# Kernel tuning notes

Hardware: AMD Instinct MI355X
Metric: run time of the kernel (lower is better)

## Reference

```python
import jax, jax.numpy as jnp
import numpy as np

B, S, D, NH = 4, 2048, 512, 8
HD = D // NH
SCALING = HD ** -0.5


def setup_inputs() -> dict:
    key = jax.random.key(0)
    ks = jax.random.split(key, 8)
    w_std = (2.0 / (D + D)) ** 0.5  # xavier_uniform-ish scale
    inp = {
        "query": jax.random.normal(ks[0], (B, S, D), jnp.float32),
        "key": jax.random.normal(ks[1], (B, S, D), jnp.float32),
        "value": jax.random.normal(ks[2], (B, S, D), jnp.float32),
        "key_mask": jnp.ones((B, S), dtype=bool),
        "attn_mask": jnp.tril(jnp.ones((S, S), dtype=bool)),  # causal, per docstring
        "Wq": jax.random.normal(ks[3], (D, D), jnp.float32) * w_std,
        "bq": jnp.zeros((D,), jnp.float32),
        "Wk": jax.random.normal(ks[4], (D, D), jnp.float32) * w_std,
        "bk": jnp.zeros((D,), jnp.float32),
        "Wv": jax.random.normal(ks[5], (D, D), jnp.float32) * w_std,
        "bv": jnp.zeros((D,), jnp.float32),
        "Wo": jax.random.normal(ks[6], (D, D), jnp.float32) * w_std,
        "bo": jnp.zeros((D,), jnp.float32),
    }
    return inp


def reference(query, key, value, key_mask, attn_mask, Wq, bq, Wk, bk, Wv, bv, Wo, bo):
    b, q_len, d = query.shape
    k_len = key.shape[1]
    # projections (nn.Linear: x @ W.T + b)
    q = (query @ Wq.T + bq) * SCALING
    k = key @ Wk.T + bk
    v = value @ Wv.T + bv
    q = q.reshape(b, q_len, NH, HD)
    k = k.reshape(b, k_len, NH, HD)
    v = v.reshape(b, k_len, NH, HD)
    # scores: [b, q, k, n]
    attn = jnp.einsum('bqnh,bknh->bqkn', q, k)
    # key_mask: 1 = attend; masked_fill(~mask, -inf)
    attn = jnp.where(key_mask[:, None, :, None], attn, -jnp.inf)
    # attn_mask: [q, k], 1 = attend
    attn = jnp.where(attn_mask[None, :, :, None], attn, -jnp.inf)
    attn = jax.nn.softmax(attn, axis=2)
    # dropout p=0.0 in eval -> identity
    out = jnp.einsum('bqkn,bknh->bqnh', attn, v)
    out = out.reshape(b, q_len, d)
    out = out @ Wo.T + bo
    return (out, attn)
```

## Files before the change

kernel.cpp:

```cpp
#include <hip/hip_runtime.h>


typedef short bf8 __attribute__((ext_vector_type(8)));
typedef short bf4 __attribute__((ext_vector_type(4)));
typedef float f4  __attribute__((ext_vector_type(4)));

#define MFMA16(a, b, c) __builtin_amdgcn_mfma_f32_16x16x32_bf16(a, b, c, 0, 0, 0)

static __device__ __forceinline__ short f2bf(float x) {
  unsigned u = __builtin_bit_cast(unsigned, x);
  unsigned r = (u + 0x7fffu + ((u >> 16) & 1u)) >> 16;
  return (short)r;
}
static __device__ __forceinline__ f4 zero4() { f4 z = {0.f, 0.f, 0.f, 0.f}; return z; }

template <int MODE, int INBF>
__global__ __launch_bounds__(256, 2) void gemm_proj(const void* __restrict__ Ain,
                                                    const float* __restrict__ W,
                                                    const float* __restrict__ bias,
                                                    void* __restrict__ outp, float scale) {
  __shared__ short As[128 * 40];
  __shared__ short Bs[128 * 40];
  const int tid = threadIdx.x;
  const int wave = tid >> 6, lane = tid & 63, quad = lane >> 4, col = lane & 15;
  const int m0 = blockIdx.y * 128, n0 = blockIdx.x * 128;
  const int row_off = (wave >> 1) * 64, col_off = (wave & 1) * 64;

  f4 acc[4][4];
#pragma unroll
  for (int i = 0; i < 4; ++i)
#pragma unroll
    for (int j = 0; j < 4; ++j) acc[i][j] = zero4();

  float bv[4];
#pragma unroll
  for (int nt = 0; nt < 4; ++nt) bv[nt] = bias[n0 + col_off + nt * 16 + col];

  for (int k0 = 0; k0 < 512; k0 += 32) {
#pragma unroll
    for (int i = 0; i < 4; ++i) {
      int c = i * 256 + tid;
      int r = c >> 3, cc = (c & 7) * 4;
      if constexpr (INBF) {
        const short* A = (const short*)Ain;
        *(bf4*)&As[r * 40 + cc] = *(const bf4*)(A + (size_t)(m0 + r) * 512 + k0 + cc);
      } else {
        const float* A = (const float*)Ain;
        f4 v = *(const f4*)(A + (size_t)(m0 + r) * 512 + k0 + cc);
        bf4 s = {f2bf(v[0]), f2bf(v[1]), f2bf(v[2]), f2bf(v[3])};
        *(bf4*)&As[r * 40 + cc] = s;
      }
      f4 w = *(const f4*)(W + (size_t)(n0 + r) * 512 + k0 + cc);
      bf4 sw = {f2bf(w[0]), f2bf(w[1]), f2bf(w[2]), f2bf(w[3])};
      *(bf4*)&Bs[r * 40 + cc] = sw;
    }
    __syncthreads();
    bf8 af[4], bw[4];
#pragma unroll
    for (int mt = 0; mt < 4; ++mt) af[mt] = *(const bf8*)&As[(row_off + mt * 16 + col) * 40 + quad * 8];
#pragma unroll
    for (int nt = 0; nt < 4; ++nt) bw[nt] = *(const bf8*)&Bs[(col_off + nt * 16 + col) * 40 + quad * 8];
#pragma unroll
    for (int mt = 0; mt < 4; ++mt)
#pragma unroll
      for (int nt = 0; nt < 4; ++nt) acc[mt][nt] = MFMA16(af[mt], bw[nt], acc[mt][nt]);
    __syncthreads();
  }

  if constexpr (MODE == 2) {
    float* out = (float*)outp;
#pragma unroll
    for (int mt = 0; mt < 4; ++mt)
#pragma unroll
      for (int nt = 0; nt < 4; ++nt) {
        int rb = m0 + row_off + mt * 16 + quad * 4;
        int cg = n0 + col_off + nt * 16 + col;
#pragma unroll
        for (int r = 0; r < 4; ++r) out[(size_t)(rb + r) * 512 + cg] = acc[mt][nt][r] + bv[nt];
      }
  } else {
    __shared__ short Ct[128 * 136];
#pragma unroll
    for (int mt = 0; mt < 4; ++mt)
#pragma unroll
      for (int nt = 0; nt < 4; ++nt) {
        if constexpr (MODE == 0) {
#pragma unroll
          for (int r = 0; r < 4; ++r)
            Ct[(row_off + mt * 16 + quad * 4 + r) * 136 + col_off + nt * 16 + col] =
                f2bf((acc[mt][nt][r] + bv[nt]) * scale);
        } else {
          bf4 s = {f2bf((acc[mt][nt][0] + bv[nt]) * scale), f2bf((acc[mt][nt][1] + bv[nt]) * scale),
                   f2bf((acc[mt][nt][2] + bv[nt]) * scale), f2bf((acc[mt][nt][3] + bv[nt]) * scale)};
          *(bf4*)&Ct[(col_off + nt * 16 + col) * 136 + row_off + mt * 16 + quad * 4] = s;
        }
      }
    __syncthreads();
    short* out = (short*)outp;
#pragma unroll
    for (int it = 0; it < 8; ++it) {
      int c = it * 256 + tid;
      if constexpr (MODE == 0) {
        int row = c >> 4, ch = (c & 15) * 8;
        int m = m0 + row, bb = m >> 11, sidx = m & 2047;
        int cg = n0 + ch, n = cg >> 6, h = cg & 63;
        bf8 v = *(const bf8*)&Ct[row * 136 + ch];
        *(bf8*)(out + ((size_t)((bb * 8 + n) * 2048 + sidx)) * 64 + h) = v;
      } else {
        int j = c >> 4, sc8 = (c & 15) * 8;
        int cg = n0 + j, n = cg >> 6, h = cg & 63;
        int m = m0 + sc8, bb = m >> 11, srow = m & 2047;
        bf8 v = *(const bf8*)&Ct[j * 136 + sc8];
        *(bf8*)(out + ((size_t)((bb * 8 + n) * 64 + h)) * 2048 + srow) = v;
      }
    }
  }
}

__global__ __launch_bounds__(512, 4) void attn_k(const short* __restrict__ Q,
                                                 const short* __restrict__ K,
                                                 const short* __restrict__ Vt,
                                                 short* __restrict__ O,
                                                 float* __restrict__ attn) {
  __shared__ float Pl[16 * 516];
  const int tid = threadIdx.x;
  const int wv = tid >> 6, lane = tid & 63, quad = lane >> 4, col = lane & 15;
  const int bid = blockIdx.x;
  const int b = bid & 3;
  const int q0 = (127 - (bid >> 2)) * 16;
  const int q_hi = q0 + 15;
  const int nsteps = (q_hi >> 6) + 1;

  const size_t hb = (size_t)(b * 8 + wv) * 2048;
  const bf8 aq0 = *(const bf8*)(Q + (hb + q0 + col) * 64 + quad * 8);
  const bf8 aq1 = *(const bf8*)(Q + (hb + q0 + col) * 64 + 32 + quad * 8);

  float rl[4] = {0.f, 0.f, 0.f, 0.f};

  for (int ks = 0; ks < nsteps; ++ks) {
    int k0 = ks << 6;
#pragma unroll
    for (int kt = 0; kt < 4; ++kt) {
      int kb = k0 + kt * 16;
      if (kb <= q_hi) {
        const short* kp = K + (hb + kb + col) * 64 + quad * 8;
        bf8 b0 = *(const bf8*)kp;
        bf8 b1 = *(const bf8*)(kp + 32);
        f4 sc = zero4();
        sc = MFMA16(aq0, b0, sc);
        sc = MFMA16(aq1, b1, sc);
        if (kb + 15 <= q0) {
#pragma unroll
          for (int r = 0; r < 4; ++r) rl[r] += __expf(sc[r]);
        } else {
          int kg = kb + col;
#pragma unroll
          for (int r = 0; r < 4; ++r) rl[r] += (kg <= q0 + quad * 4 + r) ? __expf(sc[r]) : 0.f;
        }
      }
    }
  }
#pragma unroll
  for (int r = 0; r < 4; ++r) {
    float v = rl[r];
    v += __shfl_xor(v, 1);
    v += __shfl_xor(v, 2);
    v += __shfl_xor(v, 4);
    v += __shfl_xor(v, 8);
    rl[r] = 1.0f / v;
  }

  f4 oacc[4];
#pragma unroll
  for (int t = 0; t < 4; ++t) oacc[t] = zero4();

  for (int ks = 0; ks < nsteps; ++ks) {
    int k0 = ks << 6;
#pragma unroll
    for (int kt = 0; kt < 4; ++kt) {
      int kb = k0 + kt * 16;
      f4 p = zero4();
      if (kb <= q_hi) {
        const short* kp = K + (hb + kb + col) * 64 + quad * 8;
        bf8 b0 = *(const bf8*)kp;
        bf8 b1 = *(const bf8*)(kp + 32);
        f4 sc = zero4();
        sc = MFMA16(aq0, b0, sc);
        sc = MFMA16(aq1, b1, sc);
        if (kb + 15 <= q0) {
#pragma unroll
          for (int r = 0; r < 4; ++r) p[r] = __expf(sc[r]) * rl[r];
        } else {
          int kg = kb + col;
#pragma unroll
          for (int r = 0; r < 4; ++r)
            p[r] = (kg <= q0 + quad * 4 + r) ? __expf(sc[r]) * rl[r] : 0.f;
        }
      }
      int kl = kt * 16 + col;
#pragma unroll
      for (int r = 0; r < 4; ++r) Pl[(quad * 4 + r) * 516 + kl * 8 + wv] = p[r];
    }
    __syncthreads();
    {
      int q = tid >> 5, c0 = tid & 31;
      float* dst = attn + ((size_t)(b * 2048 + q0 + q) * 2048 + k0) * 8;
      const float* src = Pl + q * 516;
#pragma unroll
      for (int i = 0; i < 4; ++i) {
        int cc = (c0 + 32 * i) * 4;
        *(f4*)(dst + cc) = *(const f4*)(src + cc);
      }
    }
#pragma unroll
    for (int kk = 0; kk < 2; ++kk) {
      const float* pp = Pl + col * 516 + (kk * 32 + quad * 8) * 8 + wv;
      bf8 ap;
#pragma unroll
      for (int j = 0; j < 8; ++j) ap[j] = f2bf(pp[j * 8]);
#pragma unroll
      for (int t = 0; t < 4; ++t) {
        const short* vp = Vt + ((size_t)((b * 8 + wv) * 64 + t * 16 + col)) * 2048 + k0 + kk * 32 + quad * 8;
        bf8 bvv = *(const bf8*)vp;
        oacc[t] = MFMA16(ap, bvv, oacc[t]);
      }
    }
    __syncthreads();
  }

  int klim = nsteps << 6;
  if (klim < 2048) {
    int nf4 = (2048 - klim) * 2;
#pragma unroll 1
    for (int qq = 0; qq < 16; ++qq) {
      f4* dst = (f4*)(attn + ((size_t)(b * 2048 + q0 + qq) * 2048 + klim) * 8);
      for (int i = tid; i < nf4; i += 512) dst[i] = zero4();
    }
  }

#pragma unroll
  for (int t = 0; t < 4; ++t)
#pragma unroll
    for (int r = 0; r < 4; ++r) Pl[(quad * 4 + r) * 516 + wv * 64 + t * 16 + col] = oacc[t][r];
  __syncthreads();
  {
    int q = tid >> 5, c0 = tid & 31;
    const float* src = Pl + q * 516;
    short* dst = O + (size_t)(b * 2048 + q0 + q) * 512;
#pragma unroll
    for (int i = 0; i < 4; ++i) {
      int cc = (c0 + 32 * i) * 4;
      f4 v = *(const f4*)(src + cc);
      bf4 s = {f2bf(v[0]), f2bf(v[1]), f2bf(v[2]), f2bf(v[3])};
      *(bf4*)(dst + cc) = s;
    }
  }
}

extern "C" void kernel_launch(void* const* d_in, const int* in_sizes, int n_in,
                              void* d_out, int out_size, void* d_ws, size_t ws_size,
                              hipStream_t stream) {
  const float* query = (const float*)d_in[0];
  const float* key = (const float*)d_in[1];
  const float* value = (const float*)d_in[2];
  const float* Wq = (const float*)d_in[5];
  const float* bq = (const float*)d_in[6];
  const float* Wk = (const float*)d_in[7];
  const float* bk = (const float*)d_in[8];
  const float* Wv = (const float*)d_in[9];
  const float* bv = (const float*)d_in[10];
  const float* Wo = (const float*)d_in[11];
  const float* bo = (const float*)d_in[12];

  char* ws = (char*)d_ws;
  const size_t MB8 = (size_t)8 * 1024 * 1024;
  short* Qb = (short*)(ws);
  short* Kb = (short*)(ws + MB8);
  short* Vt = (short*)(ws + 2 * MB8);
  short* Ob = (short*)(ws + 3 * MB8);

  float* out = (float*)d_out;
  float* attn = out + (size_t)4 * 2048 * 512;

  dim3 g(4, 64);
  gemm_proj<0, 0><<<g, 256, 0, stream>>>((const void*)query, Wq, bq, (void*)Qb, 0.125f);
  gemm_proj<0, 0><<<g, 256, 0, stream>>>((const void*)key, Wk, bk, (void*)Kb, 1.0f);
  gemm_proj<1, 0><<<g, 256, 0, stream>>>((const void*)value, Wv, bv, (void*)Vt, 1.0f);
  attn_k<<<512, 512, 0, stream>>>(Qb, Kb, Vt, Ob, attn);
  gemm_proj<2, 1><<<g, 256, 0, stream>>>((const void*)Ob, Wo, bo, (void*)out, 1.0f);
}
```

Measured before the change: 883.4 us.

## Batch QKV projections into one launch and restructure attention P staging layout

Merges the three Q/K/V projection GEMMs into a single launch using blockIdx.z, giving one larger grid instead of three small sequential kernels. In the attention kernel, P is now staged per-head in padded LDS slabs, so the MFMA A-operand can be read with vector loads. Softmax normalisation is moved out of the inner loop: it is applied to the attention-probability store and to the final output accumulator. The huge attention-probability tensor is written with nontemporal stores. The new LDS layout makes the global write gather across slabs, which may cause bank conflicts, and adds a shared array for the reciprocal row sums.

```diff
diff --git a/kernel.cpp b/kernel.cpp
--- a/kernel.cpp
+++ b/kernel.cpp
@@ -14,11 +14,111 @@
 }
 static __device__ __forceinline__ f4 zero4() { f4 z = {0.f, 0.f, 0.f, 0.f}; return z; }
 
-template <int MODE, int INBF>
-__global__ __launch_bounds__(256, 2) void gemm_proj(const void* __restrict__ Ain,
-                                                    const float* __restrict__ W,
-                                                    const float* __restrict__ bias,
-                                                    void* __restrict__ outp, float scale) {
+__global__ __launch_bounds__(256, 3) void gemm_qkv(const float* __restrict__ Aq,
+                                                   const float* __restrict__ Ak,
+                                                   const float* __restrict__ Av,
+                                                   const float* __restrict__ Wq,
+                                                   const float* __restrict__ Wk,
+                                                   const float* __restrict__ Wv,
+                                                   const float* __restrict__ bq,
+                                                   const float* __restrict__ bk,
+                                                   const float* __restrict__ bv,
+                                                   short* __restrict__ Qo,
+                                                   short* __restrict__ Ko,
+                                                   short* __restrict__ Vo) {
+  __shared__ short As[128 * 40];
+  __shared__ short Bs[128 * 40];
+  const int z = blockIdx.z;
+  const float* A = (z == 0) ? Aq : (z == 1) ? Ak : Av;
+  const float* W = (z == 0) ? Wq : (z == 1) ? Wk : Wv;
+  const float* bias = (z == 0) ? bq : (z == 1) ? bk : bv;
+  short* out = (z == 0) ? Qo : (z == 1) ? Ko : Vo;
+  const float scale = (z == 0) ? 0.125f : 1.0f;
+
+  const int tid = threadIdx.x;
+  const int wave = tid >> 6, lane = tid & 63, quad = lane >> 4, col = lane & 15;
+  const int m0 = blockIdx.y * 128, n0 = blockIdx.x * 128;
+  const int row_off = (wave >> 1) * 64, col_off = (wave & 1) * 64;
+
+  f4 acc[4][4];
+#pragma unroll
+  for (int i = 0; i < 4; ++i)
+#pragma unroll
+    for (int j = 0; j < 4; ++j) acc[i][j] = zero4();
+
+  float bvv[4];
+#pragma unroll
+  for (int nt = 0; nt < 4; ++nt) bvv[nt] = bias[n0 + col_off + nt * 16 + col];
+
+  for (int k0 = 0; k0 < 512; k0 += 32) {
+#pragma unroll
+    for (int i = 0; i < 4; ++i) {
+      int c = i * 256 + tid;
+      int r = c >> 3, cc = (c & 7) * 4;
+      f4 v = *(const f4*)(A + (size_t)(m0 + r) * 512 + k0 + cc);
+      bf4 s = {f2bf(v[0]), f2bf(v[1]), f2bf(v[2]), f2bf(v[3])};
+      *(bf4*)&As[r * 40 + cc] = s;
+      f4 w = *(const f4*)(W + (size_t)(n0 + r) * 512 + k0 + cc);
+      bf4 sw = {f2bf(w[0]), f2bf(w[1]), f2bf(w[2]), f2bf(w[3])};
+      *(bf4*)&Bs[r * 40 + cc] = sw;
+    }
+    __syncthreads();
+    bf8 af[4], bw[4];
+#pragma unroll
+    for (int mt = 0; mt < 4; ++mt) af[mt] = *(const bf8*)&As[(row_off + mt * 16 + col) * 40 + quad * 8];
+#pragma unroll
+    for (int nt = 0; nt < 4; ++nt) bw[nt] = *(const bf8*)&Bs[(col_off + nt * 16 + col) * 40 + quad * 8];
+#pragma unroll
+    for (int mt = 0; mt < 4; ++mt)
+#pragma unroll
+      for (int nt = 0; nt < 4; ++nt) acc[mt][nt] = MFMA16(af[mt], bw[nt], acc[mt][nt]);
+    __syncthreads();
+  }
+
+  __shared__ short Ct[128 * 136];
+  if (z != 2) {
+#pragma unroll
+    for (int mt = 0; mt < 4; ++mt)
+#pragma unroll
+      for (int nt = 0; nt < 4; ++nt)
+#pragma unroll
+        for (int r = 0; r < 4; ++r)
+          Ct[(row_off + mt * 16 + quad * 4 + r) * 136 + col_off + nt * 16 + col] =
+              f2bf((acc[mt][nt][r] + bvv[nt]) * scale);
+  } else {
+#pragma unroll
+    for (int mt = 0; mt < 4; ++mt)
+#pragma unroll
+      for (int nt = 0; nt < 4; ++nt) {
+        bf4 s = {f2bf(acc[mt][nt][0] + bvv[nt]), f2bf(acc[mt][nt][1] + bvv[nt]),
+                 f2bf(acc[mt][nt][2] + bvv[nt]), f2bf(acc[mt][nt][3] + bvv[nt])};
+        *(bf4*)&Ct[(col_off + nt * 16 + col) * 136 + row_off + mt * 16 + quad * 4] = s;
+      }
+  }
+  __syncthreads();
+#pragma unroll
+  for (int it = 0; it < 8; ++it) {
+    int c = it * 256 + tid;
+    if (z != 2) {
+      int row = c >> 4, ch = (c & 15) * 8;
+      int m = m0 + row, bb = m >> 11, sidx = m & 2047;
+      int cg = n0 + ch, n = cg >> 6, h = cg & 63;
+      bf8 v = *(const bf8*)&Ct[row * 136 + ch];
+      *(bf8*)(out + ((size_t)((bb * 8 + n) * 2048 + sidx)) * 64 + h) = v;
+    } else {
+      int j = c >> 4, sc8 = (c & 15) * 8;
+      int cg = n0 + j, n = cg >> 6, h = cg & 63;
+      int m = m0 + sc8, bb = m >> 11, srow = m & 2047;
+      bf8 v = *(const bf8*)&Ct[j * 136 + sc8];
+      *(bf8*)(out + ((size_t)((bb * 8 + n) * 64 + h)) * 2048 + srow) = v;
+    }
+  }
+}
+
+__global__ __launch_bounds__(256, 2) void gemm_out(const short* __restrict__ A,
+                                                   const float* __restrict__ W,
+                                                   const float* __restrict__ bias,
+                                                   float* __restrict__ out) {
   __shared__ short As[128 * 40];
   __shared__ short Bs[128 * 40];
   const int tid = threadIdx.x;
@@ -41,15 +141,7 @@
     for (int i = 0; i < 4; ++i) {
       int c = i * 256 + tid;
       int r = c >> 3, cc = (c & 7) * 4;
-      if constexpr (INBF) {
-        const short* A = (const short*)Ain;
-        *(bf4*)&As[r * 40 + cc] = *(const bf4*)(A + (size_t)(m0 + r) * 512 + k0 + cc);
-      } else {
-        const float* A = (const float*)Ain;
-        f4 v = *(const f4*)(A + (size_t)(m0 + r) * 512 + k0 + cc);
-        bf4 s = {f2bf(v[0]), f2bf(v[1]), f2bf(v[2]), f2bf(v[3])};
-        *(bf4*)&As[r * 40 + cc] = s;
-      }
+      *(bf4*)&As[r * 40 + cc] = *(const bf4*)(A + (size_t)(m0 + r) * 512 + k0 + cc);
       f4 w = *(const f4*)(W + (size_t)(n0 + r) * 512 + k0 + cc);
       bf4 sw = {f2bf(w[0]), f2bf(w[1]), f2bf(w[2]), f2bf(w[3])};
       *(bf4*)&Bs[r * 40 + cc] = sw;
@@ -67,62 +159,26 @@
     __syncthreads();
   }
 
-  if constexpr (MODE == 2) {
-    float* out = (float*)outp;
-#pragma unroll
-    for (int mt = 0; mt < 4; ++mt)
-#pragma unroll
-      for (int nt = 0; nt < 4; ++nt) {
-        int rb = m0 + row_off + mt * 16 + quad * 4;
-        int cg = n0 + col_off + nt * 16 + col;
-#pragma unroll
-        for (int r = 0; r < 4; ++r) out[(size_t)(rb + r) * 512 + cg] = acc[mt][nt][r] + bv[nt];
-      }
-  } else {
-    __shared__ short Ct[128 * 136];
-#pragma unroll
-    for (int mt = 0; mt < 4; ++mt)
-#pragma unroll
-      for (int nt = 0; nt < 4; ++nt) {
-        if constexpr (MODE == 0) {
-#pragma unroll
-          for (int r = 0; r < 4; ++r)
-            Ct[(row_off + mt * 16 + quad * 4 + r) * 136 + col_off + nt * 16 + col] =
-                f2bf((acc[mt][nt][r] + bv[nt]) * scale);
-        } else {
-          bf4 s = {f2bf((acc[mt][nt][0] + bv[nt]) * scale), f2bf((acc[mt][nt][1] + bv[nt]) * scale),
-                   f2bf((acc[mt][nt][2] + bv[nt]) * scale), f2bf((acc[mt][nt][3] + bv[nt]) * scale)};
-          *(bf4*)&Ct[(col_off + nt * 16 + col) * 136 + row_off + mt * 16 + quad * 4] = s;
-        }
-      }
-    __syncthreads();
-    short* out = (short*)outp;
-#pragma unroll
-    for (int it = 0; it < 8; ++it) {
-      int c = it * 256 + tid;
-      if constexpr (MODE == 0) {
-        int row = c >> 4, ch = (c & 15) * 8;
-        int m = m0 + row, bb = m >> 11, sidx = m & 2047;
-        int cg = n0 + ch, n = cg >> 6, h = cg & 63;
-        bf8 v = *(const bf8*)&Ct[row * 136 + ch];
-        *(bf8*)(out + ((size_t)((bb * 8 + n) * 2048 + sidx)) * 64 + h) = v;
-      } else {
-        int j = c >> 4, sc8 = (c & 15) * 8;
-        int cg = n0 + j, n = cg >> 6, h = cg & 63;
-        int m = m0 + sc8, bb = m >> 11, srow = m & 2047;
-        bf8 v = *(const bf8*)&Ct[j * 136 + sc8];
-        *(bf8*)(out + ((size_t)((bb * 8 + n) * 64 + h)) * 2048 + srow) = v;
-      }
-    }
-  }
-}
+#pragma unroll
+  for (int mt = 0; mt < 4; ++mt)
+#pragma unroll
+    for (int nt = 0; nt < 4; ++nt) {
+      int rb = m0 + row_off + mt * 16 + quad * 4;
+      int cg = n0 + col_off + nt * 16 + col;
+#pragma unroll
+      for (int r = 0; r < 4; ++r) out[(size_t)(rb + r) * 512 + cg] = acc[mt][nt][r] + bv[nt];
+    }
+}
+
+#define SLAB 1092
 
 __global__ __launch_bounds__(512, 4) void attn_k(const short* __restrict__ Q,
                                                  const short* __restrict__ K,
                                                  const short* __restrict__ Vt,
                                                  short* __restrict__ O,
                                                  float* __restrict__ attn) {
-  __shared__ float Pl[16 * 516];
+  __shared__ float Pl[8 * SLAB];
+  __shared__ float rl_s[128];
   const int tid = threadIdx.x;
   const int wv = tid >> 6, lane = tid & 63, quad = lane >> 4, col = lane & 15;
   const int bid = blockIdx.x;
@@ -136,7 +192,6 @@
   const bf8 aq1 = *(const bf8*)(Q + (hb + q0 + col) * 64 + 32 + quad * 8);
 
   float rl[4] = {0.f, 0.f, 0.f, 0.f};
-
   for (int ks = 0; ks < nsteps; ++ks) {
     int k0 = ks << 6;
 #pragma unroll
@@ -169,6 +224,17 @@
     v += __shfl_xor(v, 8);
     rl[r] = 1.0f / v;
   }
+  if (col == 0) {
+#pragma unroll
+    for (int r = 0; r < 4; ++r) rl_s[wv * 16 + quad * 4 + r] = rl[r];
+  }
+  __syncthreads();
+
+  const int gq = tid >> 5, gc0 = tid & 31;
+  const int gnb = (gc0 & 1) * 4, gk0 = gc0 >> 1;
+  float rl8[4];
+#pragma unroll
+  for (int j = 0; j < 4; ++j) rl8[j] = rl_s[(gnb + j) * 16 + gq];
 
   f4 oacc[4];
 #pragma unroll
@@ -189,35 +255,37 @@
         sc = MFMA16(aq1, b1, sc);
         if (kb + 15 <= q0) {
 #pragma unroll
-          for (int r = 0; r < 4; ++r) p[r] = __expf(sc[r]) * rl[r];
+          for (int r = 0; r < 4; ++r) p[r] = __expf(sc[r]);
         } else {
           int kg = kb + col;
 #pragma unroll
-          for (int r = 0; r < 4; ++r)
-            p[r] = (kg <= q0 + quad * 4 + r) ? __expf(sc[r]) * rl[r] : 0.f;
+          for (int r = 0; r < 4; ++r) p[r] = (kg <= q0 + quad * 4 + r) ? __expf(sc[r]) : 0.f;
         }
       }
-      int kl = kt * 16 + col;
-#pragma unroll
-      for (int r = 0; r < 4; ++r) Pl[(quad * 4 + r) * 516 + kl * 8 + wv] = p[r];
+      float* wp = Pl + wv * SLAB + (quad * 4) * 68 + kt * 16 + col;
+#pragma unroll
+      for (int r = 0; r < 4; ++r) wp[r * 68] = p[r];
     }
     __syncthreads();
     {
-      int q = tid >> 5, c0 = tid & 31;
-      float* dst = attn + ((size_t)(b * 2048 + q0 + q) * 2048 + k0) * 8;
-      const float* src = Pl + q * 516;
+      float* dst = attn + ((size_t)(b * 2048 + q0 + gq) * 2048 + k0) * 8;
+      const float* base = Pl + gq * 68;
 #pragma unroll
       for (int i = 0; i < 4; ++i) {
-        int cc = (c0 + 32 * i) * 4;
-        *(f4*)(dst + cc) = *(const f4*)(src + cc);
+        int k = gk0 + 16 * i;
+        f4 v;
+#pragma unroll
+        for (int j = 0; j < 4; ++j) v[j] = base[(gnb + j) * SLAB + k] * rl8[j];
+        __builtin_nontemporal_store(v, (f4*)(dst + k * 8 + gnb));
       }
     }
 #pragma unroll
     for (int kk = 0; kk < 2; ++kk) {
-      const float* pp = Pl + col * 516 + (kk * 32 + quad * 8) * 8 + wv;
-      bf8 ap;
-#pragma unroll
-      for (int j = 0; j < 8; ++j) ap[j] = f2bf(pp[j * 8]);
+      const float* pp = Pl + wv * SLAB + col * 68 + kk * 32 + quad * 8;
+      f4 a0 = *(const f4*)pp;
+      f4 a1 = *(const f4*)(pp + 4);
+      bf8 ap = {f2bf(a0[0]), f2bf(a0[1]), f2bf(a0[2]), f2bf(a0[3]),
+                f2bf(a1[0]), f2bf(a1[1]), f2bf(a1[2]), f2bf(a1[3])};
 #pragma unroll
       for (int t = 0; t < 4; ++t) {
         const short* vp = Vt + ((size_t)((b * 8 + wv) * 64 + t * 16 + col)) * 2048 + k0 + kk * 32 + quad * 8;
@@ -234,22 +302,22 @@
 #pragma unroll 1
     for (int qq = 0; qq < 16; ++qq) {
       f4* dst = (f4*)(attn + ((size_t)(b * 2048 + q0 + qq) * 2048 + klim) * 8);
-      for (int i = tid; i < nf4; i += 512) dst[i] = zero4();
+      for (int i = tid; i < nf4; i += 512) __builtin_nontemporal_store(zero4(), dst + i);
     }
   }
 
 #pragma unroll
   for (int t = 0; t < 4; ++t)
 #pragma unroll
-    for (int r = 0; r < 4; ++r) Pl[(quad * 4 + r) * 516 + wv * 64 + t * 16 + col] = oacc[t][r];
+    for (int r = 0; r < 4; ++r)
+      Pl[(quad * 4 + r) * 516 + wv * 64 + t * 16 + col] = oacc[t][r] * rl[r];
   __syncthreads();
   {
-    int q = tid >> 5, c0 = tid & 31;
-    const float* src = Pl + q * 516;
-    short* dst = O + (size_t)(b * 2048 + q0 + q) * 512;
+    const float* src = Pl + gq * 516;
+    short* dst = O + (size_t)(b * 2048 + q0 + gq) * 512;
 #pragma unroll
     for (int i = 0; i < 4; ++i) {
-      int cc = (c0 + 32 * i) * 4;
+      int cc = (gc0 + 32 * i) * 4;
       f4 v = *(const f4*)(src + cc);
       bf4 s = {f2bf(v[0]), f2bf(v[1]), f2bf(v[2]), f2bf(v[3])};
       *(bf4*)(dst + cc) = s;
@@ -282,10 +350,7 @@
   float* out = (float*)d_out;
   float* attn = out + (size_t)4 * 2048 * 512;
 
-  dim3 g(4, 64);
-  gemm_proj<0, 0><<<g, 256, 0, stream>>>((const void*)query, Wq, bq, (void*)Qb, 0.125f);
-  gemm_proj<0, 0><<<g, 256, 0, stream>>>((const void*)key, Wk, bk, (void*)Kb, 1.0f);
-  gemm_proj<1, 0><<<g, 256, 0, stream>>>((const void*)value, Wv, bv, (void*)Vt, 1.0f);
+  gemm_qkv<<<dim3(4, 64, 3), 256, 0, stream>>>(query, key, value, Wq, Wk, Wv, bq, bk, bv, Qb, Kb, Vt);
   attn_k<<<512, 512, 0, stream>>>(Qb, Kb, Vt, Ob, attn);
-  gemm_proj<2, 1><<<g, 256, 0, stream>>>((const void*)Ob, Wo, bo, (void*)out, 1.0f);
-}
+  gemm_out<<<dim3(4, 64), 256, 0, stream>>>(Ob, Wo, bo, out);
+}
```

New measurement: 832.4 us. 5.8% less time.
